# Performance work log

Measured on AMD Instinct MI355X. Metric: run time of the kernel, lower is better.

The kernel has to match this reference:

```python
import jax, jax.numpy as jnp
import numpy as np

B, T, C, H, D, W = 4, 4096, 1024, 16, 64, 128  # batch, seq, n_embd, n_head, head_dim, window
NB = T // W  # number of query blocks
EPS = 1e-6


def _rms(x, w):
    # RMSNorm over last dim
    return x * jax.lax.rsqrt(jnp.mean(x * x, axis=-1, keepdims=True) + EPS) * w


def _rope(x, pos_ids):
    # MRoPE: pos_ids [T,3]; axis_id maps each freq to one of 3 axes
    inv_freq = 1.0 / (1e6 ** (jnp.arange(0, D, 2, dtype=jnp.float32) / D))  # [D/2]
    axis_id = jnp.arange(D // 2) % 3
    positions = pos_ids[:, axis_id].astype(jnp.float32)  # [T, D/2]
    freqs = positions * inv_freq  # [T, D/2]
    emb = jnp.concatenate([freqs, freqs], axis=-1)  # [T, D]
    cos = jnp.cos(emb)[None, None]  # [1,1,T,D]
    sin = jnp.sin(emb)[None, None]
    x1, x2 = x[..., : D // 2], x[..., D // 2 :]
    rot = jnp.concatenate([-x2, x1], axis=-1)
    return x * cos + rot * sin


def setup_inputs() -> dict:
    key = jax.random.key(0)
    ks = jax.random.split(key, 3)
    x = jax.random.normal(ks[0], (B, T, C), jnp.float32)
    pos = jnp.arange(T, dtype=jnp.int32)
    pos_ids = jnp.stack([pos, pos, pos], axis=-1)  # [T,3] text positions
    w_attn = jax.random.normal(ks[1], (C, C + 2 * D), jnp.float32) * 0.02
    w_proj = jax.random.normal(ks[2], (C, C), jnp.float32) * 0.02
    q_norm_w = jnp.ones((D,), jnp.float32)
    k_norm_w = jnp.ones((D,), jnp.float32)
    return {"x": x, "pos_ids": pos_ids, "w_attn": w_attn, "w_proj": w_proj,
            "q_norm_w": q_norm_w, "k_norm_w": k_norm_w}


def reference(x, pos_ids, w_attn, w_proj, q_norm_w, k_norm_w):
    # fused qkv projection (torch Linear without bias; weight stored [in,out])
    qkv = x @ w_attn  # [B,T,C+2D]
    q = qkv[..., :C].reshape(B, T, H, D).transpose(0, 2, 1, 3)  # [B,H,T,D]
    k = qkv[..., C : C + D][:, None]  # [B,1,T,D] single KV head (MQA)
    v = qkv[..., C + D :][:, None]  # [B,1,T,D]
    q = _rope(_rms(q, q_norm_w), pos_ids)
    k = _rope(_rms(k, k_norm_w), pos_ids)
    # sliding-window attention (q >= kv and q - kv <= W), computed in blocks of W
    qb = q.reshape(B, H, NB, W, D)
    kb = k.reshape(B, NB, W, D)
    vb = v.reshape(B, NB, W, D)
    kp = jnp.concatenate([jnp.zeros_like(kb[:, :1]), kb[:, :-1]], axis=1)  # prev k block
    vp = jnp.concatenate([jnp.zeros_like(vb[:, :1]), vb[:, :-1]], axis=1)
    kv_k = jnp.concatenate([kp, kb], axis=2)  # [B,NB,2W,D]
    kv_v = jnp.concatenate([vp, vb], axis=2)
    n = jnp.arange(NB)[:, None, None]
    qr = jnp.arange(W)[None, :, None]
    kr = jnp.arange(2 * W)[None, None, :]
    q_abs = n * W + qr
    kv_abs = (n - 1) * W + kr
    mask = (q_abs >= kv_abs) & (q_abs - kv_abs <= W) & (kv_abs >= 0)  # [NB,W,2W]
    scores = jnp.einsum("bhnqd,bnkd->bhnqk", qb, kv_k) / jnp.sqrt(jnp.float32(D))
    scores = jnp.where(mask[None, None], scores, -1e30)
    attn = jax.nn.softmax(scores, axis=-1)
    y = jnp.einsum("bhnqk,bnkd->bhnqd", attn, kv_v)  # [B,H,NB,W,D]
    y = y.reshape(B, H, T, D).transpose(0, 2, 1, 3).reshape(B, T, C)
    return y @ w_proj
```

## Files before the change

### kernel.cpp

```cpp
#include <hip/hip_runtime.h>


typedef __attribute__((ext_vector_type(8))) short short8;
typedef __attribute__((ext_vector_type(4))) float f32x4;
typedef __attribute__((ext_vector_type(16))) float f32x16;
typedef __attribute__((ext_vector_type(4))) unsigned uint4v;

#define DEV static __device__ __forceinline__

DEV unsigned short f2bf(float f) {
  unsigned u = __builtin_bit_cast(unsigned, f);
  u += 0x7fffu + ((u >> 16) & 1u);
  return (unsigned short)(u >> 16);
}
DEV float bf2f(unsigned short s) {
  unsigned u = ((unsigned)s) << 16;
  return __builtin_bit_cast(float, u);
}
DEV unsigned cvtpk(float a, float b) {
  unsigned r;
  asm("v_cvt_pk_bf16_f32 %0, %1, %2" : "=v"(r) : "v"(a), "v"(b));
  return r;
}

DEV f32x4 mfma16(short8 a, short8 b, f32x4 c) {
  return __builtin_amdgcn_mfma_f32_16x16x32_bf16(a, b, c, 0, 0, 0);
}
DEV f32x16 mfma32(short8 a, short8 b, f32x16 c) {
  return __builtin_amdgcn_mfma_f32_32x32x16_bf16(a, b, c, 0, 0, 0);
}

DEV void gload16(const void* g, void* l) {
  __builtin_amdgcn_global_load_lds(
      (const __attribute__((address_space(1))) unsigned int*)(unsigned long long)g,
      (__attribute__((address_space(3))) unsigned int*)(unsigned int)(unsigned long long)l,
      16, 0, 0);
}

#define BARRIER __builtin_amdgcn_s_barrier()
#define LGKM0  asm volatile("s_waitcnt lgkmcnt(0)" ::: "memory")
#define VMCNT4 asm volatile("s_waitcnt vmcnt(4)" ::: "memory")

__global__ __launch_bounds__(256) void k_cvt(const float* __restrict__ in,
                                             short* __restrict__ out, int n4) {
  int i = blockIdx.x * 256 + threadIdx.x;
  if (i >= n4) return;
  float4 v = ((const float4*)in)[i];
  short4 o;
  o.x = (short)f2bf(v.x); o.y = (short)f2bf(v.y);
  o.z = (short)f2bf(v.z); o.w = (short)f2bf(v.w);
  ((short4*)out)[i] = o;
}

__global__ __launch_bounds__(256) void k_tcvt(const float* __restrict__ W,
                                              short* __restrict__ Wt, int K, int N) {
  __shared__ float tl[32][33];
  int tx = threadIdx.x & 31, ty = threadIdx.x >> 5;
  int k0 = blockIdx.x * 32, n0 = blockIdx.y * 32;
#pragma unroll
  for (int i = 0; i < 4; ++i)
    tl[ty + i * 8][tx] = W[(size_t)(k0 + ty + i * 8) * N + n0 + tx];
  __syncthreads();
#pragma unroll
  for (int i = 0; i < 4; ++i)
    Wt[(size_t)(n0 + ty + i * 8) * K + k0 + tx] = (short)f2bf(tl[tx][ty + i * 8]);
}

__global__ __launch_bounds__(256) void k_trig(const int* __restrict__ pos,
                                              float* __restrict__ tbl) {
  int idx = blockIdx.x * 256 + threadIdx.x;
  int t = idx >> 5, j = idx & 31;
  float invf = __expf((float)j * (-13.815510558f / 32.f));
  float p = (float)pos[t * 3 + (j % 3)];
  float s, c;
  sincosf(p * invf, &s, &c);
  ((float2*)tbl)[idx] = make_float2(c, s);
}

__global__ __launch_bounds__(256) void k_gemmkv(const short* __restrict__ A,
                                                const short* __restrict__ Bt,
                                                const float* __restrict__ trig,
                                                const float* __restrict__ kw,
                                                short* __restrict__ kb2,
                                                short* __restrict__ vtg) {
  __shared__ short As[128 * 32];
  __shared__ short Bs[128 * 32];
  const int K = 1024;
  int bid = blockIdx.x;
  int bm = (bid & 7) * 16 + (bid >> 3);
  int tid = threadIdx.x, lane = tid & 63, wid = tid >> 6;
  int wr = wid >> 1, wc = wid & 1;
  int lo = lane & 15, hi = lane >> 4;
  const short* Ab = A + (size_t)(bm * 128 + (tid >> 2)) * K + (tid & 3) * 8;
  const short* Bb = Bt + (size_t)(tid >> 2) * K + (tid & 3) * 8;
  f32x4 acc[4][4] = {};
  for (int kt = 0; kt < K; kt += 32) {
    gload16(Ab + kt,            As + tid * 8);
    gload16(Ab + kt + 64 * K,   As + 2048 + tid * 8);
    gload16(Bb + kt,            Bs + tid * 8);
    gload16(Bb + kt + 64 * K,   Bs + 2048 + tid * 8);
    __syncthreads();
    short8 a[4], b[4];
#pragma unroll
    for (int m = 0; m < 4; ++m)
      a[m] = *(const short8*)&As[(wr * 64 + m * 16 + lo) * 32 + hi * 8];
#pragma unroll
    for (int n = 0; n < 4; ++n)
      b[n] = *(const short8*)&Bs[(wc * 64 + n * 16 + lo) * 32 + hi * 8];
#pragma unroll
    for (int m = 0; m < 4; ++m)
#pragma unroll
      for (int n = 0; n < 4; ++n)
        acc[m][n] = mfma16(a[m], b[n], acc[m][n]);
    __syncthreads();
  }
  int tg0 = (bm * 128 + wr * 64) & 4095;
  int bb  = (bm * 128) >> 12;
  if (wc == 0) {
    float w0 = kw[lo], w1 = kw[16 + lo], w2 = kw[32 + lo], w3 = kw[48 + lo];
    const float2* tb = (const float2*)trig;
#pragma unroll
    for (int m = 0; m < 4; ++m)
#pragma unroll
      for (int r = 0; r < 4; ++r) {
        float x0 = acc[m][0][r], x1 = acc[m][1][r];
        float x2 = acc[m][2][r], x3 = acc[m][3][r];
        float ss = x0 * x0 + x1 * x1 + x2 * x2 + x3 * x3;
        ss += __shfl_xor(ss, 1); ss += __shfl_xor(ss, 2);
        ss += __shfl_xor(ss, 4); ss += __shfl_xor(ss, 8);
        float rn = rsqrtf(ss * 0.015625f + 1e-6f);
        x0 *= rn * w0; x1 *= rn * w1; x2 *= rn * w2; x3 *= rn * w3;
        int tp = tg0 + m * 16 + hi * 4 + r;
        float2 cs0 = tb[tp * 32 + lo];
        float2 cs1 = tb[tp * 32 + 16 + lo];
        float o0 = x0 * cs0.x - x2 * cs0.y;
        float o1 = x1 * cs1.x - x3 * cs1.y;
        float o2 = x2 * cs0.x + x0 * cs0.y;
        float o3 = x3 * cs1.x + x1 * cs1.y;
        size_t tb_ = ((size_t)bb * 4096 + tp) * 64;
        kb2[tb_ + lo]      = (short)f2bf(o0);
        kb2[tb_ + 16 + lo] = (short)f2bf(o1);
        kb2[tb_ + 32 + lo] = (short)f2bf(o2);
        kb2[tb_ + 48 + lo] = (short)f2bf(o3);
      }
  } else {
#pragma unroll
    for (int m = 0; m < 4; ++m)
#pragma unroll
      for (int nf = 0; nf < 4; ++nf) {
        int dd = nf * 16 + lo;
        short4 o;
        o.x = (short)f2bf(acc[m][nf][0]);
        o.y = (short)f2bf(acc[m][nf][1]);
        o.z = (short)f2bf(acc[m][nf][2]);
        o.w = (short)f2bf(acc[m][nf][3]);
        *(short4*)&vtg[((size_t)(bb * 64 + dd)) * 4096 + tg0 + m * 16 + hi * 4] = o;
      }
  }
}

__global__ __launch_bounds__(512, 2) void k_gemm256(
    const short* __restrict__ A, const short* __restrict__ Bt,
    void* __restrict__ Cout, int M, int N, int K, int outBf16,
    const float* __restrict__ trig, const float* __restrict__ qw,
    short* __restrict__ qb2, int mode) {
  __shared__ short sm[65536];
  int nbn = N >> 8;
  int nwg = (M >> 8) * nbn;
  int bid = blockIdx.x;
  int swz = (bid & 7) * (nwg >> 3) + (bid >> 3);
  int bm = swz / nbn, bn = swz % nbn;
  int tid = threadIdx.x, wid = tid >> 6, lane = tid & 63;
  int wm = wid >> 2, wn = wid & 3;
  int lo = lane & 15, hi = lane >> 4;
  int NT = K >> 6;

  int r0 = tid >> 3, dc = tid & 7;
  int sc = dc ^ (r0 & 7);
  const short* aS0 = A  + (size_t)(bm * 256 + r0) * K + sc * 8;
  const short* bS0 = Bt + (size_t)(bn * 256 + r0) * K + sc * 8;
  size_t hstep = (size_t)128 * K;

  auto stage = [&](int jt, int mat, int h, int d) {
    const short* s = (mat ? bS0 : aS0) + (size_t)h * hstep + jt * 64;
    short* l = sm + d * 32768 + mat * 16384 + h * 8192;
    gload16(s,                     l + tid * 8);
    gload16(s + (size_t)64 * K,    l + 4096 + tid * 8);
  };

  int aRd[2];
#pragma unroll
  for (int kk = 0; kk < 2; ++kk)
    aRd[kk] = lo * 64 + (((kk << 2) | hi) ^ (lo & 7)) * 8;

  short8 Afr[8][2];
  short8 Bfr[2][2];
  f32x4 acc[8][4] = {};

  auto rdA = [&](int d, int m0) {
    int base = d * 32768 + wm * 8192;
#pragma unroll
    for (int m = 0; m < 4; ++m)
#pragma unroll
      for (int kk = 0; kk < 2; ++kk)
        Afr[m0 + m][kk] = *(const short8*)&sm[base + (m0 + m) * 1024 + aRd[kk]];
  };
  auto rdB = [&](int d, int n0) {
    int base = d * 32768 + 16384 + (wn >> 1) * 8192 + (wn & 1) * 4096;
#pragma unroll
    for (int nf = 0; nf < 2; ++nf)
#pragma unroll
      for (int kk = 0; kk < 2; ++kk)
        Bfr[nf][kk] = *(const short8*)&sm[base + (n0 + nf) * 1024 + aRd[kk]];
  };
  auto quad = [&](int m0, int n0) {
    __builtin_amdgcn_s_setprio(1);
#pragma unroll
    for (int m = 0; m < 4; ++m)
#pragma unroll
      for (int j = 0; j < 2; ++j)
#pragma unroll
        for (int kk = 0; kk < 2; ++kk)
          acc[m0 + m][n0 + j] = mfma16(Afr[m0 + m][kk], Bfr[j][kk], acc[m0 + m][n0 + j]);
    __builtin_amdgcn_s_setprio(0);
  };

  stage(0, 0, 0, 0); stage(0, 1, 0, 0); stage(0, 0, 1, 0); stage(0, 1, 1, 0);
  if (NT > 1) { stage(1, 0, 0, 1); stage(1, 1, 0, 1); }
  VMCNT4;
  BARRIER;

#pragma unroll 2
  for (int jt = 0; jt < NT; ++jt) {
    int d = jt & 1;
    rdA(d, 0); rdB(d, 0);
    if (jt + 1 < NT) stage(jt + 1, 0, 1, d ^ 1);
    BARRIER; LGKM0;
    quad(0, 0);
    BARRIER;
    rdA(d, 4);
    if (jt + 1 < NT) stage(jt + 1, 1, 1, d ^ 1);
    BARRIER; LGKM0;
    quad(4, 0);
    BARRIER;
    rdB(d, 2);
    if (jt + 2 < NT) stage(jt + 2, 0, 0, d);
    BARRIER; LGKM0;
    quad(0, 2);
    BARRIER;
    if (jt + 2 < NT) stage(jt + 2, 1, 0, d);
    VMCNT4;
    BARRIER;
    quad(4, 2);
    BARRIER;
  }

  if (mode == 1) {
    int tg0 = (bm * 256 + wm * 128) & 4095;
    int bb  = (bm * 256) >> 12;
    int hh  = bn * 4 + wn;
    float w0 = qw[lo], w1 = qw[16 + lo], w2 = qw[32 + lo], w3 = qw[48 + lo];
    short* dst = qb2 + (size_t)((bb * 16 + hh) * 4096) * 64;
    const float2* tb = (const float2*)trig;
#pragma unroll
    for (int m = 0; m < 8; ++m)
#pragma unroll
      for (int r = 0; r < 4; ++r) {
        float x0 = acc[m][0][r], x1 = acc[m][1][r];
        float x2 = acc[m][2][r], x3 = acc[m][3][r];
        float ss = x0 * x0 + x1 * x1 + x2 * x2 + x3 * x3;
        ss += __shfl_xor(ss, 1); ss += __shfl_xor(ss, 2);
        ss += __shfl_xor(ss, 4); ss += __shfl_xor(ss, 8);
        float rn = rsqrtf(ss * 0.015625f + 1e-6f);
        x0 *= rn * w0; x1 *= rn * w1; x2 *= rn * w2; x3 *= rn * w3;
        int tp = tg0 + m * 16 + hi * 4 + r;
        float2 cs0 = tb[tp * 32 + lo];
        float2 cs1 = tb[tp * 32 + 16 + lo];
        float o0 = x0 * cs0.x - x2 * cs0.y;
        float o1 = x1 * cs1.x - x3 * cs1.y;
        float o2 = x2 * cs0.x + x0 * cs0.y;
        float o3 = x3 * cs1.x + x1 * cs1.y;
        size_t tb_ = (size_t)tp * 64;
        dst[tb_ + lo]      = (short)f2bf(o0);
        dst[tb_ + 16 + lo] = (short)f2bf(o1);
        dst[tb_ + 32 + lo] = (short)f2bf(o2);
        dst[tb_ + 48 + lo] = (short)f2bf(o3);
      }
    return;
  }

  int row0 = bm * 256 + wm * 128 + hi * 4;
  int col0 = bn * 256 + wn * 64 + lo;
  if (outBf16) {
    short* C = (short*)Cout;
#pragma unroll
    for (int m = 0; m < 8; ++m)
#pragma unroll
      for (int nf = 0; nf < 4; ++nf)
#pragma unroll
        for (int r = 0; r < 4; ++r)
          C[(size_t)(row0 + m * 16 + r) * N + col0 + nf * 16] = (short)f2bf(acc[m][nf][r]);
  } else {
    float* C = (float*)Cout;
#pragma unroll
    for (int m = 0; m < 8; ++m)
#pragma unroll
      for (int nf = 0; nf < 4; ++nf)
#pragma unroll
        for (int r = 0; r < 4; ++r)
          C[(size_t)(row0 + m * 16 + r) * N + col0 + nf * 16] = acc[m][nf][r];
  }
}

__global__ __launch_bounds__(256, 4) void k_attn(const short* __restrict__ qb,
                                                 const short* __restrict__ kb,
                                                 const short* __restrict__ vtg,
                                                 short* __restrict__ y) {
  __shared__ __align__(16) char smem[33792];
  short* ks  = (short*)smem;
  short* vts = (short*)(smem + 16384);
  int bid = blockIdx.x;
  int swz = (bid & 7) * 256 + (bid >> 3);
  int h = swz & 15, n = (swz >> 4) & 31, b = swz >> 9;
  int tid = threadIdx.x, wid = tid >> 6, lane = tid & 63;
  int lo = lane & 31, hi = lane >> 5;

  const short* qrow = qb + (size_t)((b * 16 + h) * 4096 + n * 128 + wid * 32 + lo) * 64;
  short8 aq[4];
#pragma unroll
  for (int s = 0; s < 4; ++s) aq[s] = *(const short8*)(qrow + s * 16 + hi * 8);

  f32x16 O0 = {}, O1 = {};
  float mrun = -1e30f, lrun = 0.f;
  int qr = wid * 32 + lo;
  const float SC = 0.125f * 1.4426950408889634f;

  for (int hf = (n == 0) ? 1 : 0; hf < 2; ++hf) {
    int tg = (n - 1 + hf) * 128;
#pragma unroll
    for (int p = 0; p < 4; ++p) {
      int idx = p * 256 + tid;
      int r = idx >> 3, dc = idx & 7;
      gload16(kb + (size_t)(b * 4096 + tg + r) * 64 + ((dc ^ (r & 7)) << 3),
              ks + idx * 8);
    }
#pragma unroll
    for (int p = 0; p < 4; ++p) {
      int idx = p * 256 + tid;
      int dd = idx >> 4, s = idx & 15;
      gload16(vtg + (size_t)(b * 64 + dd) * 4096 + tg + ((s ^ (dd & 7)) << 3),
              vts + idx * 8);
    }
    __syncthreads();

#pragma unroll
    for (int mt = 0; mt < 4; ++mt) {
      f32x16 S = {};
      int r = mt * 32 + lo;
#pragma unroll
      for (int kst = 0; kst < 4; ++kst) {
        short8 kf = *(const short8*)&ks[r * 64 + ((((kst << 1) | hi) ^ (r & 7)) << 3)];
        S = mfma32(kf, aq[kst], S);
      }
#pragma unroll
      for (int rr = 0; rr < 16; ++rr) {
        int kg = hf * 128 + mt * 32 + (rr & 3) + ((rr >> 2) << 3) + (hi << 2);
        S[rr] = (kg >= qr && kg <= qr + 128) ? S[rr] * SC : -30000.f;
      }
      float pmax = S[0];
#pragma unroll
      for (int rr = 1; rr < 16; ++rr) pmax = fmaxf(pmax, S[rr]);
      pmax = fmaxf(pmax, __shfl_xor(pmax, 32));
      if (!__all(pmax - mrun <= 8.f)) {
        float mn = fmaxf(mrun, pmax);
        float al = exp2f(mrun - mn);
        lrun *= al; mrun = mn;
#pragma unroll
        for (int rr = 0; rr < 16; ++rr) { O0[rr] *= al; O1[rr] *= al; }
      }
      float ls = 0.f;
#pragma unroll
      for (int rr = 0; rr < 16; ++rr) { S[rr] = exp2f(S[rr] - mrun); ls += S[rr]; }
      ls += __shfl_xor(ls, 32);
      lrun += ls;
#pragma unroll
      for (int h2 = 0; h2 < 2; ++h2) {
        int b0 = h2 * 8;
        unsigned pk0 = cvtpk(S[b0 + 0], S[b0 + 1]);
        unsigned pk1 = cvtpk(S[b0 + 2], S[b0 + 3]);
        unsigned pk2 = cvtpk(S[b0 + 4], S[b0 + 5]);
        unsigned pk3 = cvtpk(S[b0 + 6], S[b0 + 7]);
        asm("v_permlane32_swap_b32 %0, %1" : "+v"(pk0), "+v"(pk2));
        asm("v_permlane32_swap_b32 %0, %1" : "+v"(pk1), "+v"(pk3));
        uint4v uw; uw.x = pk0; uw.y = pk1; uw.z = pk2; uw.w = pk3;
        short8 pb = __builtin_bit_cast(short8, uw);
        int kc = mt * 4 + h2 * 2 + hi;
        short8 vb0 = *(const short8*)&vts[lo * 128 + ((kc ^ (lo & 7)) << 3)];
        short8 vb1 = *(const short8*)&vts[(32 + lo) * 128 + ((kc ^ (lo & 7)) << 3)];
        O0 = mfma32(vb0, pb, O0);
        O1 = mfma32(vb1, pb, O1);
      }
    }
    __syncthreads();
  }

  float inv = 1.f / lrun;
  float* ot = (float*)smem + wid * 2112;
#pragma unroll
  for (int r = 0; r < 16; ++r) {
    int d0 = (r & 3) + ((r >> 2) << 3) + (hi << 2);
    ot[d0 * 33 + lo]        = O0[r] * inv;
    ot[(d0 + 32) * 33 + lo] = O1[r] * inv;
  }
  __syncthreads();
  int tok = lane >> 3, dc = lane & 7;
#pragma unroll
  for (int g = 0; g < 4; ++g) {
    int q = g * 8 + tok;
    short8 o8;
#pragma unroll
    for (int jj = 0; jj < 8; ++jj)
      o8[jj] = (short)f2bf(ot[(dc * 8 + jj) * 33 + q]);
    *(short8*)&y[(size_t)(b * 4096 + n * 128 + wid * 32 + q) * 1024 + h * 64 + dc * 8] = o8;
  }
}

extern "C" void kernel_launch(void* const* d_in, const int* in_sizes, int n_in,
                              void* d_out, int out_size, void* d_ws, size_t ws_size,
                              hipStream_t stream) {
  const float* x      = (const float*)d_in[0];
  const int*   pos    = (const int*)d_in[1];
  const float* w_attn = (const float*)d_in[2];
  const float* w_proj = (const float*)d_in[3];
  const float* qw     = (const float*)d_in[4];
  const float* kw     = (const float*)d_in[5];

  char* ws = (char*)d_ws;
  short* xb   = (short*)ws;
  short* wabt = (short*)(ws + 33554432);
  short* wpbt = (short*)(ws + 35913728);
  short* qb2  = (short*)(ws + 38010880);
  short* kb2  = (short*)(ws + 71565312);
  short* vtg  = (short*)(ws + 73662464);
  float* trig = (float*)(ws + 75759616);
  short* ybuf = xb;

  hipLaunchKernelGGL(k_cvt, dim3(16384), dim3(256), 0, stream, x, xb, 4194304);
  hipLaunchKernelGGL(k_tcvt, dim3(32, 36), dim3(256), 0, stream, w_attn, wabt, 1024, 1152);
  hipLaunchKernelGGL(k_tcvt, dim3(32, 32), dim3(256), 0, stream, w_proj, wpbt, 1024, 1024);
  hipLaunchKernelGGL(k_trig, dim3(512), dim3(256), 0, stream, pos, trig);
  hipLaunchKernelGGL(k_gemmkv, dim3(128), dim3(256), 0, stream, xb,
                     wabt + (size_t)1024 * 1024, trig, kw, kb2, vtg);
  hipLaunchKernelGGL(k_gemm256, dim3(256), dim3(512), 0, stream, xb, wabt,
                     (void*)nullptr, 16384, 1024, 1024, 1, trig, qw, qb2, 1);
  hipLaunchKernelGGL(k_attn, dim3(2048), dim3(256), 0, stream, qb2, kb2, vtg, ybuf);
  hipLaunchKernelGGL(k_gemm256, dim3(256), dim3(512), 0, stream, ybuf, wpbt, d_out,
                     16384, 1024, 1024, 0,
                     (const float*)nullptr, (const float*)nullptr,
                     (short*)nullptr, 0);
}
```

Baseline: 167.7 us.

## Merge prep kernels and simplify GEMM pipeline to full-tile double buffering

Fuses the bf16 conversion, weight transpose and trig-table kernels into one launch dispatched by block index, removing three kernel launches. Replaces the 256x256 GEMM's fine-grained interleaved half-tile staging, with its explicit vmcnt/lgkm waits and many barriers, with whole-tile double buffering: it prefetches the next K tile, computes all four quadrants, then does one __syncthreads per iteration. This cuts barrier count but loses the finer overlap of loads with MFMA work and raises register use for B fragments.

```diff
diff --git a/kernel.cpp b/kernel.cpp
--- a/kernel.cpp
+++ b/kernel.cpp
@@ -37,44 +37,49 @@
       16, 0, 0);
 }
 
-#define BARRIER __builtin_amdgcn_s_barrier()
-#define LGKM0  asm volatile("s_waitcnt lgkmcnt(0)" ::: "memory")
-#define VMCNT4 asm volatile("s_waitcnt vmcnt(4)" ::: "memory")
-
-__global__ __launch_bounds__(256) void k_cvt(const float* __restrict__ in,
-                                             short* __restrict__ out, int n4) {
-  int i = blockIdx.x * 256 + threadIdx.x;
-  if (i >= n4) return;
-  float4 v = ((const float4*)in)[i];
-  short4 o;
-  o.x = (short)f2bf(v.x); o.y = (short)f2bf(v.y);
-  o.z = (short)f2bf(v.z); o.w = (short)f2bf(v.w);
-  ((short4*)out)[i] = o;
-}
-
-__global__ __launch_bounds__(256) void k_tcvt(const float* __restrict__ W,
-                                              short* __restrict__ Wt, int K, int N) {
+__global__ __launch_bounds__(256) void k_prep(const float* __restrict__ x,
+                                              short* __restrict__ xb,
+                                              const float* __restrict__ wa,
+                                              short* __restrict__ wabt,
+                                              const float* __restrict__ wp,
+                                              short* __restrict__ wpbt,
+                                              const int* __restrict__ pos,
+                                              float* __restrict__ trig) {
   __shared__ float tl[32][33];
-  int tx = threadIdx.x & 31, ty = threadIdx.x >> 5;
-  int k0 = blockIdx.x * 32, n0 = blockIdx.y * 32;
-#pragma unroll
-  for (int i = 0; i < 4; ++i)
-    tl[ty + i * 8][tx] = W[(size_t)(k0 + ty + i * 8) * N + n0 + tx];
-  __syncthreads();
-#pragma unroll
-  for (int i = 0; i < 4; ++i)
-    Wt[(size_t)(n0 + ty + i * 8) * K + k0 + tx] = (short)f2bf(tl[tx][ty + i * 8]);
-}
-
-__global__ __launch_bounds__(256) void k_trig(const int* __restrict__ pos,
-                                              float* __restrict__ tbl) {
-  int idx = blockIdx.x * 256 + threadIdx.x;
-  int t = idx >> 5, j = idx & 31;
-  float invf = __expf((float)j * (-13.815510558f / 32.f));
-  float p = (float)pos[t * 3 + (j % 3)];
-  float s, c;
-  sincosf(p * invf, &s, &c);
-  ((float2*)tbl)[idx] = make_float2(c, s);
+  int bid = blockIdx.x, tid = threadIdx.x;
+  if (bid < 16384) {
+    int i = bid * 256 + tid;
+    float4 v = ((const float4*)x)[i];
+    short4 o;
+    o.x = (short)f2bf(v.x); o.y = (short)f2bf(v.y);
+    o.z = (short)f2bf(v.z); o.w = (short)f2bf(v.w);
+    ((short4*)xb)[i] = o;
+    return;
+  }
+  if (bid < 16384 + 1152 + 1024) {
+    const float* W; short* Wt; int N, local;
+    if (bid < 16384 + 1152) { local = bid - 16384; W = wa; Wt = wabt; N = 1152; }
+    else { local = bid - 16384 - 1152; W = wp; Wt = wpbt; N = 1024; }
+    int k0 = (local & 31) * 32, n0 = (local >> 5) * 32;
+    int tx = tid & 31, ty = tid >> 5;
+#pragma unroll
+    for (int i = 0; i < 4; ++i)
+      tl[ty + i * 8][tx] = W[(size_t)(k0 + ty + i * 8) * N + n0 + tx];
+    __syncthreads();
+#pragma unroll
+    for (int i = 0; i < 4; ++i)
+      Wt[(size_t)(n0 + ty + i * 8) * 1024 + k0 + tx] = (short)f2bf(tl[tx][ty + i * 8]);
+    return;
+  }
+  {
+    int idx = (bid - 16384 - 1152 - 1024) * 256 + tid;
+    int t = idx >> 5, j = idx & 31;
+    float invf = __expf((float)j * (-13.815510558f / 32.f));
+    float p = (float)pos[t * 3 + (j % 3)];
+    float s, c;
+    sincosf(p * invf, &s, &c);
+    ((float2*)trig)[idx] = make_float2(c, s);
+  }
 }
 
 __global__ __launch_bounds__(256) void k_gemmkv(const short* __restrict__ A,
@@ -181,11 +186,16 @@
   const short* bS0 = Bt + (size_t)(bn * 256 + r0) * K + sc * 8;
   size_t hstep = (size_t)128 * K;
 
-  auto stage = [&](int jt, int mat, int h, int d) {
-    const short* s = (mat ? bS0 : aS0) + (size_t)h * hstep + jt * 64;
-    short* l = sm + d * 32768 + mat * 16384 + h * 8192;
-    gload16(s,                     l + tid * 8);
-    gload16(s + (size_t)64 * K,    l + 4096 + tid * 8);
+  auto stageAll = [&](int jt, int d) {
+#pragma unroll
+    for (int mat = 0; mat < 2; ++mat)
+#pragma unroll
+      for (int h = 0; h < 2; ++h) {
+        const short* s = (mat ? bS0 : aS0) + (size_t)h * hstep + jt * 64;
+        short* l = sm + d * 32768 + mat * 16384 + h * 8192;
+        gload16(s,                  l + tid * 8);
+        gload16(s + (size_t)64 * K, l + 4096 + tid * 8);
+      }
   };
 
   int aRd[2];
@@ -194,7 +204,7 @@
     aRd[kk] = lo * 64 + (((kk << 2) | hi) ^ (lo & 7)) * 8;
 
   short8 Afr[8][2];
-  short8 Bfr[2][2];
+  short8 Bfr[4][2];
   f32x4 acc[8][4] = {};
 
   auto rdA = [&](int d, int m0) {
@@ -211,7 +221,7 @@
     for (int nf = 0; nf < 2; ++nf)
 #pragma unroll
       for (int kk = 0; kk < 2; ++kk)
-        Bfr[nf][kk] = *(const short8*)&sm[base + (n0 + nf) * 1024 + aRd[kk]];
+        Bfr[n0 + nf][kk] = *(const short8*)&sm[base + (n0 + nf) * 1024 + aRd[kk]];
   };
   auto quad = [&](int m0, int n0) {
     __builtin_amdgcn_s_setprio(1);
@@ -221,38 +231,23 @@
       for (int j = 0; j < 2; ++j)
 #pragma unroll
         for (int kk = 0; kk < 2; ++kk)
-          acc[m0 + m][n0 + j] = mfma16(Afr[m0 + m][kk], Bfr[j][kk], acc[m0 + m][n0 + j]);
+          acc[m0 + m][n0 + j] = mfma16(Afr[m0 + m][kk], Bfr[n0 + j][kk],
+                                       acc[m0 + m][n0 + j]);
     __builtin_amdgcn_s_setprio(0);
   };
 
-  stage(0, 0, 0, 0); stage(0, 1, 0, 0); stage(0, 0, 1, 0); stage(0, 1, 1, 0);
-  if (NT > 1) { stage(1, 0, 0, 1); stage(1, 1, 0, 1); }
-  VMCNT4;
-  BARRIER;
+  stageAll(0, 0);
+  __syncthreads();
 
 #pragma unroll 2
   for (int jt = 0; jt < NT; ++jt) {
     int d = jt & 1;
-    rdA(d, 0); rdB(d, 0);
-    if (jt + 1 < NT) stage(jt + 1, 0, 1, d ^ 1);
-    BARRIER; LGKM0;
-    quad(0, 0);
-    BARRIER;
+    if (jt + 1 < NT) stageAll(jt + 1, d ^ 1);
+    rdA(d, 0); rdB(d, 0); rdB(d, 2);
+    quad(0, 0); quad(0, 2);
     rdA(d, 4);
-    if (jt + 1 < NT) stage(jt + 1, 1, 1, d ^ 1);
-    BARRIER; LGKM0;
-    quad(4, 0);
-    BARRIER;
-    rdB(d, 2);
-    if (jt + 2 < NT) stage(jt + 2, 0, 0, d);
-    BARRIER; LGKM0;
-    quad(0, 2);
-    BARRIER;
-    if (jt + 2 < NT) stage(jt + 2, 1, 0, d);
-    VMCNT4;
-    BARRIER;
-    quad(4, 2);
-    BARRIER;
+    quad(4, 0); quad(4, 2);
+    __syncthreads();
   }
 
   if (mode == 1) {
@@ -445,10 +440,8 @@
   float* trig = (float*)(ws + 75759616);
   short* ybuf = xb;
 
-  hipLaunchKernelGGL(k_cvt, dim3(16384), dim3(256), 0, stream, x, xb, 4194304);
-  hipLaunchKernelGGL(k_tcvt, dim3(32, 36), dim3(256), 0, stream, w_attn, wabt, 1024, 1152);
-  hipLaunchKernelGGL(k_tcvt, dim3(32, 32), dim3(256), 0, stream, w_proj, wpbt, 1024, 1024);
-  hipLaunchKernelGGL(k_trig, dim3(512), dim3(256), 0, stream, pos, trig);
+  hipLaunchKernelGGL(k_prep, dim3(16384 + 1152 + 1024 + 512), dim3(256), 0, stream,
+                     x, xb, w_attn, wabt, w_proj, wpbt, pos, trig);
   hipLaunchKernelGGL(k_gemmkv, dim3(128), dim3(256), 0, stream, xb,
                      wabt + (size_t)1024 * 1024, trig, kw, kb2, vtg);
   hipLaunchKernelGGL(k_gemm256, dim3(256), dim3(512), 0, stream, xb, wabt,
```

Result: faster. 160.2 us (-4.5%).
